# Kernel tuning notes

Measured on AMD Instinct MI355X. Metric: run time of the kernel, lower is better.

The kernel has to match this reference:

```python
import jax, jax.numpy as jnp
import numpy as np

N_NODES = 51200
N_GRAPHS = 64
NODES_PER_GRAPH = 800
N_EDGES = 819200
DIM_IN = 128
DIM_HIDDEN = 64
HEADS = 3
DIM_OUT = 64


def leaky(x, slope):
    return jnp.where(x >= 0, x, slope * x)


def setup_inputs() -> dict:
    key = jax.random.key(0)
    ks = jax.random.split(key, 12)
    s = lambda fan_in: 1.0 / np.sqrt(fan_in)
    X = jax.random.normal(ks[0], (N_NODES, DIM_IN), dtype=jnp.float32)
    edge_indices = jax.random.randint(ks[1], (2, N_EDGES), 0, N_NODES, dtype=jnp.int32)
    ptr = (jnp.arange(N_GRAPHS + 1, dtype=jnp.int32) * NODES_PER_GRAPH)
    # linearSeq: Linear(dim_in, dim_hidden) + LeakyReLU
    W1 = jax.random.uniform(ks[2], (DIM_IN, DIM_HIDDEN), jnp.float32, -s(DIM_IN), s(DIM_IN))
    b1 = jax.random.uniform(ks[3], (DIM_HIDDEN,), jnp.float32, -s(DIM_IN), s(DIM_IN))
    # GATConv params: lin_src/lin_dst (no bias), att_src/att_dst, bias (concat=False -> out_channels)
    W_src = jax.random.uniform(ks[4], (DIM_HIDDEN, HEADS * DIM_HIDDEN), jnp.float32, -s(DIM_HIDDEN), s(DIM_HIDDEN))
    W_dst = jax.random.uniform(ks[5], (DIM_HIDDEN, HEADS * DIM_HIDDEN), jnp.float32, -s(DIM_HIDDEN), s(DIM_HIDDEN))
    att_src = jax.random.normal(ks[6], (HEADS, DIM_HIDDEN), dtype=jnp.float32) * 0.1
    att_dst = jax.random.normal(ks[7], (HEADS, DIM_HIDDEN), dtype=jnp.float32) * 0.1
    gat_bias = jnp.zeros((DIM_HIDDEN,), dtype=jnp.float32)
    # linear_final: Linear(2*dim_hidden, dim_out)
    Wf = jax.random.uniform(ks[8], (2 * DIM_HIDDEN, DIM_OUT), jnp.float32, -s(2 * DIM_HIDDEN), s(2 * DIM_HIDDEN))
    bf = jax.random.uniform(ks[9], (DIM_OUT,), jnp.float32, -s(2 * DIM_HIDDEN), s(2 * DIM_HIDDEN))
    return {"X": X, "W1": W1, "b1": b1, "W_src": W_src, "W_dst": W_dst,
            "att_src": att_src, "att_dst": att_dst, "gat_bias": gat_bias,
            "Wf": Wf, "bf": bf, "edge_indices": edge_indices, "ptr": ptr}


def reference(X, W1, b1, W_src, W_dst, att_src, att_dst, gat_bias, Wf, bf, edge_indices, ptr):
    N = X.shape[0]
    src, dst = edge_indices[0], edge_indices[1]  # message flows src -> dst
    # input projection
    h = leaky(X @ W1 + b1, 0.01)                                  # [N, DH]
    # GATConv (heads=3, concat=False, add_self_loops=False)
    x_src = (h @ W_src).reshape(N, HEADS, DIM_HIDDEN)             # [N, H, C]
    x_dst = (h @ W_dst).reshape(N, HEADS, DIM_HIDDEN)
    a_src = jnp.einsum('nhc,hc->nh', x_src, att_src)              # [N, H]
    a_dst = jnp.einsum('nhc,hc->nh', x_dst, att_dst)
    logits = leaky(a_src[src] + a_dst[dst], 0.2)                  # [E, H]
    # segment softmax over incoming edges of each target node
    m = jax.ops.segment_max(logits, dst, num_segments=N)          # [N, H]
    e = jnp.exp(logits - m[dst])
    denom = jax.ops.segment_sum(e, dst, num_segments=N)           # [N, H]
    attn = e / denom[dst]                                         # [E, H]
    msg = x_src[src] * attn[..., None]                            # [E, H, C]
    agg = jax.ops.segment_sum(msg, dst, num_segments=N)           # [N, H, C]
    out = agg.mean(axis=1) + gat_bias                             # concat=False -> head mean
    # final head
    cat = jnp.concatenate([h, out], axis=1)                       # [N, 2*DH]
    y = leaky(cat, 0.01) @ Wf + bf                                # [N, DO]
    # aggregate_using_ptr: mean-pool nodes per graph using CSR ptr
    node_graph = jnp.searchsorted(ptr, jnp.arange(N), side='right') - 1
    sums = jax.ops.segment_sum(y, node_graph, num_segments=ptr.shape[0] - 1)
    counts = (ptr[1:] - ptr[:-1]).astype(y.dtype)
    pooled = sums / counts[:, None]                               # [n_graphs, DO]
    return pooled, attn
```

## Files before the change

### kernel.cpp

```cpp
#include <hip/hip_runtime.h>
#include <hip/hip_bf16.h>

#define N_NODES   51200
#define N_GRAPHS  64
#define N_EDGES   819200
#define DIM_IN    128
#define DH        64
#define HEADS     3
#define DIM_OUT   64
#define CAP       96
#define NPART     64
#define PART_SZ   (N_NODES / NPART)
#define PBUF_CAP  16384
#define BIN_BLOCKS  (N_EDGES / 2048)
#define PREP_BLOCKS 116
#define SC_BLOCKS   NPART
#define K1_BLOCKS   (N_NODES / 64)

typedef __hip_bfloat16 bf16;
typedef short bf16x8 __attribute__((ext_vector_type(8)));
typedef float f32x4  __attribute__((ext_vector_type(4)));

__device__ __forceinline__ float b2f(bf16 x) { return __bfloat162float(x); }
__device__ __forceinline__ bf16  f2b(float x) { return __float2bfloat16(x); }
__device__ __forceinline__ short f2bs(float x) { return (short)__bfloat16_as_ushort(f2b(x)); }
__device__ __forceinline__ float leaky(float x, float s) { return x >= 0.f ? x : s * x; }
__device__ __forceinline__ float ldin(const void* p, size_t i, int f32) {
    return f32 ? ((const float*)p)[i] : b2f(((const bf16*)p)[i]);
}
__device__ __forceinline__ bf16x8 ld8(const void* p, size_t i, int f32) {
    if (!f32) return *((const bf16x8*)((const short*)p + i));
    const float* f = (const float*)p + i;
    bf16x8 r;
    #pragma unroll
    for (int j = 0; j < 8; ++j) r[j] = f2bs(f[j]);
    return r;
}

__global__ __launch_bounds__(256) void k_bin_prep(const int* __restrict__ src,
                                                  const int* __restrict__ dst,
                                                  int* __restrict__ pcur,
                                                  unsigned* __restrict__ pbuf,
                                                  const void* __restrict__ X,
                                                  const void* __restrict__ W1,
                                                  const void* __restrict__ Wsrc,
                                                  const void* __restrict__ Wdst,
                                                  const void* __restrict__ Wf,
                                                  const void* __restrict__ att_src,
                                                  const void* __restrict__ att_dst,
                                                  int* __restrict__ flag,
                                                  short* __restrict__ W1t,
                                                  short* __restrict__ Wspt,
                                                  short* __restrict__ Wft,
                                                  short* __restrict__ Wat) {
    const int tid = threadIdx.x;
    if (blockIdx.x < BIN_BLOCKS) {
        __shared__ int cnt[NPART];
        __shared__ int base[NPART];
        if (tid < NPART) cnt[tid] = 0;
        __syncthreads();
        const int e0 = blockIdx.x * 2048;
        unsigned pk[8]; int pp[8]; int rr[8];
        #pragma unroll
        for (int t = 0; t < 8; ++t) {
            int e = e0 + t * 256 + tid;
            int s = src[e], d = dst[e];
            int p = d / PART_SZ;
            pk[t] = ((unsigned)s << 16) | (unsigned)d;
            pp[t] = p;
            rr[t] = atomicAdd(&cnt[p], 1);
        }
        __syncthreads();
        if (tid < NPART) base[tid] = atomicAdd(&pcur[tid], cnt[tid]);
        __syncthreads();
        #pragma unroll
        for (int t = 0; t < 8; ++t) {
            int o = base[pp[t]] + rr[t];
            if (o < PBUF_CAP) pbuf[(size_t)pp[t] * PBUF_CAP + o] = pk[t];
        }
        return;
    }
    if (blockIdx.x < BIN_BLOCKS + PREP_BLOCKS) {
        unsigned ex = (((const unsigned short*)X)[2 * tid] >> 7) & 0xFF;
        int c = __syncthreads_count(ex >= 110 && ex <= 135);
        const int f32 = (c < 128) ? 1 : 0;
        int idx = (blockIdx.x - BIN_BLOCKS) * 256 + tid;
        if (idx < 8192) {
            int n = idx >> 7, k = idx & 127;
            W1t[idx] = f2bs(ldin(W1, (size_t)k * 64 + n, f32));
        } else if (idx < 20480) {
            int j = idx - 8192;
            int col = j / 192;
            int rem = j - col * 192;
            int hh = rem >> 6, kk = rem & 63;
            Wspt[j] = f2bs(ldin(Wsrc, (size_t)kk * 192 + hh * 64 + col, f32) * (1.0f / 3.0f));
        } else if (idx < 28672) {
            int j = idx - 20480;
            int n = j >> 7, k = j & 127;
            Wft[j] = f2bs(ldin(Wf, (size_t)k * 64 + n, f32));
        } else if (idx < 29696) {
            int j = idx - 28672;
            int n = j >> 6, k = j & 63;
            float v = 0.f;
            if (n < 3) {
                for (int c2 = 0; c2 < 64; ++c2)
                    v += ldin(Wsrc, (size_t)k * 192 + n * 64 + c2, f32) * ldin(att_src, n * 64 + c2, f32);
            } else if (n < 6) {
                for (int c2 = 0; c2 < 64; ++c2)
                    v += ldin(Wdst, (size_t)k * 192 + (n - 3) * 64 + c2, f32) * ldin(att_dst, (n - 3) * 64 + c2, f32);
            }
            Wat[j] = f2bs(v);
        }
        return;
    }
    __shared__ int cntp;
    if (tid == 0) cntp = 0;
    __syncthreads();
    int local = 0;
    const unsigned short* Xu = (const unsigned short*)X;
    for (int i = tid * 2; i < 8192; i += 512) {
        unsigned e = (Xu[i] >> 7) & 0xFF;
        if (e >= 110 && e <= 135) local++;
    }
    atomicAdd(&cntp, local);
    __syncthreads();
    if (tid == 0) *flag = (cntp < 2048) ? 1 : 0;
}

__global__ __launch_bounds__(256) void k_scatter_k1(const unsigned* __restrict__ pbuf,
                                                    const int* __restrict__ pcur,
                                                    int* __restrict__ cursor,
                                                    unsigned short* __restrict__ bucket,
                                                    const void* __restrict__ X,
                                                    const short* __restrict__ W1t,
                                                    const short* __restrict__ Wat,
                                                    const void* __restrict__ b1,
                                                    const int* __restrict__ flagp,
                                                    bf16* __restrict__ h_bf,
                                                    unsigned char* __restrict__ h8,
                                                    float* __restrict__ a_src4,
                                                    float* __restrict__ a_dst4) {
    __shared__ short hs[64 * 72];
    __shared__ int cnt2[PART_SZ];
    const int tid = threadIdx.x;
    if (blockIdx.x < SC_BLOCKS) {
        const int p = blockIdx.x;
        const int nbase = p * PART_SZ;
        for (int i = tid; i < PART_SZ; i += 256) cnt2[i] = 0;
        __syncthreads();
        const int pc = min(pcur[p], PBUF_CAP);
        const unsigned* pb = pbuf + (size_t)p * PBUF_CAP;
        for (int i = tid; i < pc; i += 256) {
            unsigned pk = pb[i];
            int d = (int)(pk & 0xFFFFu);
            int pos = atomicAdd(&cnt2[d - nbase], 1);
            if (pos < CAP) bucket[(size_t)d * CAP + pos] = (unsigned short)(pk >> 16);
        }
        __syncthreads();
        for (int i = tid; i < PART_SZ; i += 256) cursor[nbase + i] = cnt2[i];
        return;
    }
    const int f32 = *flagp;
    const int w    = tid >> 6;
    const int lane = tid & 63;
    const int lm   = lane & 15;
    const int q    = lane >> 4;
    const int row0 = (blockIdx.x - SC_BLOCKS) * 64;

    const float bias = ldin(b1, w * 16 + lm, f32);
    for (int mt = 0; mt < 4; ++mt) {
        f32x4 acc = {0.f, 0.f, 0.f, 0.f};
        #pragma unroll
        for (int kc = 0; kc < 4; ++kc) {
            bf16x8 a = ld8(X, (size_t)(row0 + mt * 16 + lm) * 128 + kc * 32 + q * 8, f32);
            bf16x8 b = *((const bf16x8*)(W1t + (size_t)(w * 16 + lm) * 128 + kc * 32 + q * 8));
            acc = __builtin_amdgcn_mfma_f32_16x16x32_bf16(a, b, acc, 0, 0, 0);
        }
        #pragma unroll
        for (int r = 0; r < 4; ++r) {
            int row = mt * 16 + q * 4 + r;
            float v = leaky(acc[r] + bias, 0.01f);
            short hv = f2bs(v);
            hs[row * 72 + w * 16 + lm] = hv;
            h_bf[(size_t)(row0 + row) * 64 + w * 16 + lm] = __ushort_as_bfloat16((unsigned short)hv);
            h8[(size_t)(row0 + row) * 64 + w * 16 + lm] =
                (unsigned char)__builtin_amdgcn_cvt_pk_fp8_f32(v, 0.f, 0, false);
        }
    }
    __syncthreads();
    {
        const int mt = w;
        bf16x8 a0  = *((const bf16x8*)(hs + (mt * 16 + lm) * 72 + q * 8));
        bf16x8 a1  = *((const bf16x8*)(hs + (mt * 16 + lm) * 72 + 32 + q * 8));
        bf16x8 b0  = *((const bf16x8*)(Wat + (size_t)lm * 64 + q * 8));
        bf16x8 b1v = *((const bf16x8*)(Wat + (size_t)lm * 64 + 32 + q * 8));
        f32x4 acca = {0.f, 0.f, 0.f, 0.f};
        acca = __builtin_amdgcn_mfma_f32_16x16x32_bf16(a0, b0, acca, 0, 0, 0);
        acca = __builtin_amdgcn_mfma_f32_16x16x32_bf16(a1, b1v, acca, 0, 0, 0);
        if (lm < 6) {
            #pragma unroll
            for (int r = 0; r < 4; ++r) {
                int row = row0 + mt * 16 + q * 4 + r;
                if (lm < 3) a_src4[(size_t)row * 4 + lm] = acca[r];
                else        a_dst4[(size_t)row * 4 + (lm - 3)] = acca[r];
            }
        }
    }
}

__global__ __launch_bounds__(256) void edge_kernel(const unsigned short* __restrict__ bucket,
                                                   const int* __restrict__ cursor,
                                                   const float* __restrict__ a_src4,
                                                   const float* __restrict__ a_dst4,
                                                   const unsigned char* __restrict__ h8,
                                                   float4* __restrict__ dstinfo,
                                                   bf16* __restrict__ wagg) {
    const int lane = threadIdx.x & 63;
    const int w = threadIdx.x >> 6;
    const int n = blockIdx.x * 4 + w;
    const int dg = min(cursor[n], CAP);
    const float4 ad = ((const float4*)a_dst4)[n];
    __shared__ float4 buf[4][64];
    float den0 = 0.f, den1 = 0.f, den2 = 0.f;
    float acc0 = 0.f, acc1 = 0.f, acc2 = 0.f;
    for (int c0 = 0; c0 < dg; c0 += 64) {
        int cnt = min(64, dg - c0);
        if (lane < cnt) {
            int s = bucket[(size_t)n * CAP + c0 + lane];
            const float4 as = ((const float4*)a_src4)[s];
            float e0 = __expf(leaky(as.x + ad.x, 0.2f));
            float e1 = __expf(leaky(as.y + ad.y, 0.2f));
            float e2 = __expf(leaky(as.z + ad.z, 0.2f));
            den0 += e0; den1 += e1; den2 += e2;
            buf[w][lane] = make_float4(e0, e1, e2, __int_as_float(s));
        }
        asm volatile("s_waitcnt lgkmcnt(0)" ::: "memory");
        int j = 0;
        for (; j + 8 <= cnt; j += 8) {
            float4 r[8]; int hv[8];
            #pragma unroll
            for (int u = 0; u < 8; ++u) r[u] = buf[w][j + u];
            #pragma unroll
            for (int u = 0; u < 8; ++u)
                hv[u] = (int)h8[(((unsigned)__float_as_int(r[u].w)) << 6) | (unsigned)lane];
            #pragma unroll
            for (int u = 0; u < 8; ++u) {
                float f = __builtin_amdgcn_cvt_f32_fp8(hv[u], 0);
                acc0 += r[u].x * f; acc1 += r[u].y * f; acc2 += r[u].z * f;
            }
        }
        for (; j < cnt; ++j) {
            float4 r = buf[w][j];
            int hvv = (int)h8[(((unsigned)__float_as_int(r.w)) << 6) | (unsigned)lane];
            float f = __builtin_amdgcn_cvt_f32_fp8(hvv, 0);
            acc0 += r.x * f; acc1 += r.y * f; acc2 += r.z * f;
        }
    }
    #pragma unroll
    for (int off = 32; off >= 1; off >>= 1) {
        den0 += __shfl_xor(den0, off);
        den1 += __shfl_xor(den1, off);
        den2 += __shfl_xor(den2, off);
    }
    float inv0 = den0 > 0.f ? 1.f / den0 : 0.f;
    float inv1 = den1 > 0.f ? 1.f / den1 : 0.f;
    float inv2 = den2 > 0.f ? 1.f / den2 : 0.f;
    size_t wb = (size_t)n * 192;
    wagg[wb + lane]       = f2b(acc0 * inv0);
    wagg[wb + 64 + lane]  = f2b(acc1 * inv1);
    wagg[wb + 128 + lane] = f2b(acc2 * inv2);
    if (lane == 0) {
        dstinfo[(size_t)n * 2 + 0] = make_float4(ad.x, ad.y, ad.z, 0.f);
        dstinfo[(size_t)n * 2 + 1] = make_float4(inv0, inv1, inv2, 0.f);
    }
}

__global__ __launch_bounds__(256) void attn_g3_kernel(const int* __restrict__ src,
                                                      const int* __restrict__ dst,
                                                      const float* __restrict__ a_src4,
                                                      const float4* __restrict__ dstinfo,
                                                      const bf16* __restrict__ h_bf,
                                                      const bf16* __restrict__ wagg,
                                                      const short* __restrict__ Wspt,
                                                      const short* __restrict__ Wft,
                                                      const void* __restrict__ gat_bias,
                                                      const void* __restrict__ bfv,
                                                      const int* __restrict__ flagp,
                                                      const int* __restrict__ gptr,
                                                      float* __restrict__ psum,
                                                      int* __restrict__ done,
                                                      void* __restrict__ d_out) {
    const int f32 = *flagp;
    __shared__ short cs[64 * 136];
    __shared__ int sptr[N_GRAPHS + 1];
    __shared__ int rowg_s[64];
    __shared__ int readyg[64];
    __shared__ int nready;
    if (blockIdx.x < N_EDGES / 256) {
        int e = blockIdx.x * 256 + threadIdx.x;
        int s = src[e], d = dst[e];
        const float4 as = ((const float4*)a_src4)[s];
        const float4 ad = dstinfo[(size_t)d * 2 + 0];
        const float4 cv = dstinfo[(size_t)d * 2 + 1];
        float a0 = __expf(leaky(as.x + ad.x, 0.2f)) * cv.x;
        float a1 = __expf(leaky(as.y + ad.y, 0.2f)) * cv.y;
        float a2 = __expf(leaky(as.z + ad.z, 0.2f)) * cv.z;
        size_t o = (size_t)N_GRAPHS * DIM_OUT + (size_t)e * 3;
        if (f32) {
            float* p = (float*)d_out;
            p[o] = a0; p[o + 1] = a1; p[o + 2] = a2;
        } else {
            bf16* p = (bf16*)d_out;
            p[o] = f2b(a0); p[o + 1] = f2b(a1); p[o + 2] = f2b(a2);
        }
        return;
    }
    const int bid  = blockIdx.x - N_EDGES / 256;
    const int tid  = threadIdx.x;
    const int w    = tid >> 6;
    const int lane = tid & 63;
    const int lm   = lane & 15;
    const int q    = lane >> 4;
    const int row0 = bid * 64;
    if (tid <= N_GRAPHS) sptr[tid] = gptr[tid];
    if (tid == 0) nready = 0;
    __syncthreads();
    if (tid < 64) {
        int row = row0 + tid;
        int lo2 = 0, hi2 = N_GRAPHS;
        while (hi2 - lo2 > 1) { int mid = (lo2 + hi2) >> 1; if (sptr[mid] <= row) lo2 = mid; else hi2 = mid; }
        rowg_s[tid] = lo2;
    }
    for (int idx = tid; idx < 64 * 64; idx += 256) {
        int r = idx >> 6, k = idx & 63;
        cs[r * 136 + k] = f2bs(leaky(b2f(h_bf[(size_t)(row0 + r) * 64 + k]), 0.01f));
    }
    {
        const int col = w * 16 + lm;
        const float gb = ldin(gat_bias, col, f32);
        for (int mt = 0; mt < 4; ++mt) {
            f32x4 acc = {0.f, 0.f, 0.f, 0.f};
            #pragma unroll
            for (int kc = 0; kc < 6; ++kc) {
                bf16x8 a = *((const bf16x8*)((const short*)wagg + (size_t)(row0 + mt * 16 + lm) * 192 + kc * 32 + q * 8));
                bf16x8 b = *((const bf16x8*)(Wspt + (size_t)col * 192 + kc * 32 + q * 8));
                acc = __builtin_amdgcn_mfma_f32_16x16x32_bf16(a, b, acc, 0, 0, 0);
            }
            #pragma unroll
            for (int r = 0; r < 4; ++r) {
                int row = mt * 16 + q * 4 + r;
                cs[row * 136 + 64 + col] = f2bs(leaky(acc[r] + gb, 0.01f));
            }
        }
    }
    __syncthreads();
    {
        const int col = w * 16 + lm;
        const float bias = ldin(bfv, col, f32);
        int curg = -1; float runsum = 0.f;
        for (int mt = 0; mt < 4; ++mt) {
            f32x4 acc = {0.f, 0.f, 0.f, 0.f};
            #pragma unroll
            for (int kc = 0; kc < 4; ++kc) {
                bf16x8 a = *((const bf16x8*)(cs + (mt * 16 + lm) * 136 + kc * 32 + q * 8));
                bf16x8 b = *((const bf16x8*)(Wft + (size_t)col * 128 + kc * 32 + q * 8));
                acc = __builtin_amdgcn_mfma_f32_16x16x32_bf16(a, b, acc, 0, 0, 0);
            }
            #pragma unroll
            for (int r = 0; r < 4; ++r) {
                int lrow = mt * 16 + q * 4 + r;
                float v = acc[r] + bias;
                int g = rowg_s[lrow];
                if (g != curg) {
                    if (curg >= 0) atomicAdd(&psum[curg * 64 + col], runsum);
                    curg = g; runsum = 0.f;
                }
                runsum += v;
            }
        }
        if (curg >= 0) atomicAdd(&psum[curg * 64 + col], runsum);
    }
    __syncthreads();
    if (tid == 0) {
        int g0 = rowg_s[0], g1 = rowg_s[63];
        int nr = 0;
        for (int g = g0; g <= g1; ++g) {
            int lo = sptr[g], hi = sptr[g + 1];
            if (hi <= lo) continue;
            int expected = (hi - 1) / 64 - lo / 64 + 1;
            int old = atomicAdd(&done[g], 1);
            if (old == expected - 1) readyg[nr++] = g;
        }
        nready = nr;
    }
    __syncthreads();
    for (int i = 0; i < nready; ++i) {
        int g = readyg[i];
        if (tid < 64) {
            float s = atomicAdd(&psum[g * 64 + tid], 0.0f);
            float v = s / (float)(sptr[g + 1] - sptr[g]);
            if (f32) ((float*)d_out)[g * DIM_OUT + tid] = v;
            else     ((bf16*)d_out)[g * DIM_OUT + tid]  = f2b(v);
        }
    }
}

extern "C" void kernel_launch(void* const* d_in, const int* in_sizes, int n_in,
                              void* d_out, int out_size, void* d_ws, size_t ws_size,
                              hipStream_t stream) {
    const void* X        = d_in[0];
    const void* W1       = d_in[1];
    const void* b1       = d_in[2];
    const void* Wsrc     = d_in[3];
    const void* Wdst     = d_in[4];
    const void* att_src  = d_in[5];
    const void* att_dst  = d_in[6];
    const void* gat_bias = d_in[7];
    const void* Wf       = d_in[8];
    const void* bfv      = d_in[9];
    const int*  ei       = (const int*)d_in[10];
    const int*  ptr      = (const int*)d_in[11];
    const int*  src  = ei;
    const int*  dstp = ei + N_EDGES;

    char* ws = (char*)d_ws;
    size_t off_b = 0;
    auto alloc = [&](size_t bytes) -> char* {
        char* p = ws + off_b;
        off_b += (bytes + 255) & ~(size_t)255;
        return p;
    };
    int*     flag    = (int*)    alloc(256);
    short*   W1t     = (short*)  alloc(8192 * 2);
    short*   Wspt    = (short*)  alloc(12288 * 2);
    short*   Wft     = (short*)  alloc(8192 * 2);
    short*   Wat     = (short*)  alloc(1024 * 2);
    bf16*    h_bf    = (bf16*)   alloc((size_t)N_NODES * 64 * 2);
    unsigned char* h8 = (unsigned char*)alloc((size_t)N_NODES * 64);
    float*   a_src4  = (float*)  alloc((size_t)N_NODES * 16);
    float*   a_dst4  = (float*)  alloc((size_t)N_NODES * 16);
    float4*  dstinfo = (float4*) alloc((size_t)N_NODES * 2 * 16);
    bf16*    wagg    = (bf16*)   alloc((size_t)N_NODES * 192 * 2);
    int*     pcur    = (int*)    alloc(256);
    float*   psum    = (float*)  alloc((size_t)N_GRAPHS * 64 * 4);
    int*     done    = (int*)    alloc(256);
    int*     cursor  = (int*)    alloc((size_t)N_NODES * 4);
    unsigned short* bucket = (unsigned short*)alloc((size_t)N_NODES * CAP * 2);
    unsigned* pbuf   = (unsigned*)wagg;
    if (off_b > ws_size) return;

    hipMemsetAsync(pcur, 0, 256 + (size_t)N_GRAPHS * 64 * 4 + 256, stream);
    hipLaunchKernelGGL(k_bin_prep, dim3(BIN_BLOCKS + PREP_BLOCKS + 1), dim3(256), 0, stream,
                       src, dstp, pcur, pbuf,
                       X, W1, Wsrc, Wdst, Wf, att_src, att_dst, flag, W1t, Wspt, Wft, Wat);
    hipLaunchKernelGGL(k_scatter_k1, dim3(SC_BLOCKS + K1_BLOCKS), dim3(256), 0, stream,
                       pbuf, pcur, cursor, bucket,
                       X, W1t, Wat, b1, flag, h_bf, h8, a_src4, a_dst4);
    hipLaunchKernelGGL(edge_kernel, dim3(N_NODES / 4), dim3(256), 0, stream,
                       bucket, cursor, a_src4, a_dst4, h8, dstinfo, wagg);
    hipLaunchKernelGGL(attn_g3_kernel, dim3(N_EDGES / 256 + N_NODES / 64), dim3(256), 0, stream,
                       src, dstp, a_src4, dstinfo, h_bf, wagg, Wspt, Wft,
                       gat_bias, bfv, flag, ptr, psum, done, d_out);
}
```

Baseline: 217.0 us.

## Replace global partition atomics with fixed per-block segments in edge binning

The binning stage now has each block write its edges for each partition into a private fixed-capacity segment (SEG_CAP slots) and record the per-block count, so the global atomicAdd on partition cursors and the second pass over the edges go away. The scatter stage reads the per-block counts into shared memory and walks all segments, skipping unused slots. This removes cross-block atomic contention and one synchronisation. The risks are silent edge loss if any block ever puts more than SEG_CAP edges into one partition, and wasted reads over the padded segments.

New measurement: 231.9 us. 1.07x slower.

```diff
diff --git a/kernel.cpp b/kernel.cpp
--- a/kernel.cpp
+++ b/kernel.cpp
@@ -10,9 +10,9 @@
 #define DIM_OUT   64
 #define CAP       96
 #define NPART     64
-#define PART_SZ   (N_NODES / NPART)
-#define PBUF_CAP  16384
-#define BIN_BLOCKS  (N_EDGES / 2048)
+#define PART_SZ   800
+#define BIN_BLOCKS  400
+#define SEG_CAP   80
 #define PREP_BLOCKS 116
 #define SC_BLOCKS   NPART
 #define K1_BLOCKS   (N_NODES / 64)
@@ -39,8 +39,8 @@
 
 __global__ __launch_bounds__(256) void k_bin_prep(const int* __restrict__ src,
                                                   const int* __restrict__ dst,
-                                                  int* __restrict__ pcur,
                                                   unsigned* __restrict__ pbuf,
+                                                  int* __restrict__ bcnt,
                                                   const void* __restrict__ X,
                                                   const void* __restrict__ W1,
                                                   const void* __restrict__ Wsrc,
@@ -56,28 +56,23 @@
     const int tid = threadIdx.x;
     if (blockIdx.x < BIN_BLOCKS) {
         __shared__ int cnt[NPART];
-        __shared__ int base[NPART];
+        const int b = blockIdx.x;
         if (tid < NPART) cnt[tid] = 0;
         __syncthreads();
-        const int e0 = blockIdx.x * 2048;
-        unsigned pk[8]; int pp[8]; int rr[8];
+        const int e0 = b * 2048;
         #pragma unroll
         for (int t = 0; t < 8; ++t) {
             int e = e0 + t * 256 + tid;
             int s = src[e], d = dst[e];
             int p = d / PART_SZ;
-            pk[t] = ((unsigned)s << 16) | (unsigned)d;
-            pp[t] = p;
-            rr[t] = atomicAdd(&cnt[p], 1);
+            int dl = d - p * PART_SZ;
+            int r = atomicAdd(&cnt[p], 1);
+            if (r < SEG_CAP)
+                pbuf[((size_t)p * BIN_BLOCKS + b) * SEG_CAP + r] =
+                    ((unsigned)s << 16) | (unsigned)dl;
         }
         __syncthreads();
-        if (tid < NPART) base[tid] = atomicAdd(&pcur[tid], cnt[tid]);
-        __syncthreads();
-        #pragma unroll
-        for (int t = 0; t < 8; ++t) {
-            int o = base[pp[t]] + rr[t];
-            if (o < PBUF_CAP) pbuf[(size_t)pp[t] * PBUF_CAP + o] = pk[t];
-        }
+        if (tid < NPART) bcnt[tid * BIN_BLOCKS + b] = min(cnt[tid], SEG_CAP);
         return;
     }
     if (blockIdx.x < BIN_BLOCKS + PREP_BLOCKS) {
@@ -128,7 +123,7 @@
 }
 
 __global__ __launch_bounds__(256) void k_scatter_k1(const unsigned* __restrict__ pbuf,
-                                                    const int* __restrict__ pcur,
+                                                    const int* __restrict__ bcnt,
                                                     int* __restrict__ cursor,
                                                     unsigned short* __restrict__ bucket,
                                                     const void* __restrict__ X,
@@ -142,19 +137,24 @@
                                                     float* __restrict__ a_dst4) {
     __shared__ short hs[64 * 72];
     __shared__ int cnt2[PART_SZ];
+    __shared__ int bc[BIN_BLOCKS];
     const int tid = threadIdx.x;
     if (blockIdx.x < SC_BLOCKS) {
         const int p = blockIdx.x;
         const int nbase = p * PART_SZ;
         for (int i = tid; i < PART_SZ; i += 256) cnt2[i] = 0;
+        for (int i = tid; i < BIN_BLOCKS; i += 256) bc[i] = bcnt[p * BIN_BLOCKS + i];
         __syncthreads();
-        const int pc = min(pcur[p], PBUF_CAP);
-        const unsigned* pb = pbuf + (size_t)p * PBUF_CAP;
-        for (int i = tid; i < pc; i += 256) {
-            unsigned pk = pb[i];
-            int d = (int)(pk & 0xFFFFu);
-            int pos = atomicAdd(&cnt2[d - nbase], 1);
-            if (pos < CAP) bucket[(size_t)d * CAP + pos] = (unsigned short)(pk >> 16);
+        const unsigned* pb = pbuf + (size_t)p * BIN_BLOCKS * SEG_CAP;
+        for (int i = tid; i < BIN_BLOCKS * SEG_CAP; i += 256) {
+            int b = (unsigned)i / SEG_CAP;
+            int r = i - b * SEG_CAP;
+            if (r < bc[b]) {
+                unsigned pk = pb[i];
+                int dl = (int)(pk & 0xFFFFu);
+                int pos = atomicAdd(&cnt2[dl], 1);
+                if (pos < CAP) bucket[(size_t)(nbase + dl) * CAP + pos] = (unsigned short)(pk >> 16);
+            }
         }
         __syncthreads();
         for (int i = tid; i < PART_SZ; i += 256) cursor[nbase + i] = cnt2[i];
@@ -441,20 +441,20 @@
     float*   a_dst4  = (float*)  alloc((size_t)N_NODES * 16);
     float4*  dstinfo = (float4*) alloc((size_t)N_NODES * 2 * 16);
     bf16*    wagg    = (bf16*)   alloc((size_t)N_NODES * 192 * 2);
-    int*     pcur    = (int*)    alloc(256);
     float*   psum    = (float*)  alloc((size_t)N_GRAPHS * 64 * 4);
     int*     done    = (int*)    alloc(256);
+    int*     bcnt    = (int*)    alloc((size_t)NPART * BIN_BLOCKS * 4);
     int*     cursor  = (int*)    alloc((size_t)N_NODES * 4);
     unsigned short* bucket = (unsigned short*)alloc((size_t)N_NODES * CAP * 2);
     unsigned* pbuf   = (unsigned*)wagg;
     if (off_b > ws_size) return;
 
-    hipMemsetAsync(pcur, 0, 256 + (size_t)N_GRAPHS * 64 * 4 + 256, stream);
+    hipMemsetAsync(psum, 0, (size_t)N_GRAPHS * 64 * 4 + 256, stream);
     hipLaunchKernelGGL(k_bin_prep, dim3(BIN_BLOCKS + PREP_BLOCKS + 1), dim3(256), 0, stream,
-                       src, dstp, pcur, pbuf,
+                       src, dstp, pbuf, bcnt,
                        X, W1, Wsrc, Wdst, Wf, att_src, att_dst, flag, W1t, Wspt, Wft, Wat);
     hipLaunchKernelGGL(k_scatter_k1, dim3(SC_BLOCKS + K1_BLOCKS), dim3(256), 0, stream,
-                       pbuf, pcur, cursor, bucket,
+                       pbuf, bcnt, cursor, bucket,
                        X, W1t, Wat, b1, flag, h_bf, h8, a_src4, a_dst4);
     hipLaunchKernelGGL(edge_kernel, dim3(N_NODES / 4), dim3(256), 0, stream,
                        bucket, cursor, a_src4, a_dst4, h8, dstinfo, wagg);
```
